# Kernel tuning notes

Measured on AMD Instinct MI355X. Metric: run time of the kernel, lower is better.

The kernel has to match this reference:

```python
import jax, jax.numpy as jnp
import numpy as np

VOCAB = 1024
HIDDEN = 64
BETA = 0.25


def setup_inputs() -> dict:
    key = jax.random.key(0)
    k1, k2 = jax.random.split(key)
    inputs = jax.random.normal(k1, (32, HIDDEN, 64, 64), dtype=jnp.float32)
    # nn.Embedding weight init: uniform(-1/vocab_size, 1/vocab_size)
    codebook = jax.random.uniform(k2, (VOCAB, HIDDEN), dtype=jnp.float32,
                                  minval=-1.0 / VOCAB, maxval=1.0 / VOCAB)
    return {"inputs": inputs, "codebook": codebook}


def reference(inputs, codebook):
    # NCHW -> NHWC
    x = jnp.transpose(inputs, (0, 2, 3, 1))  # [B,H,W,C]
    flat = x.reshape(-1, HIDDEN)             # [N,C]
    # squared L2 distances via the matmul expansion (as in the original)
    distances = (jnp.sum(flat ** 2, axis=1, keepdims=True)
                 + jnp.sum(codebook ** 2, axis=1)
                 - 2.0 * flat @ codebook.T)  # [N,V]
    idx = jnp.argmin(distances, axis=1)      # [N]
    one_hot = jax.nn.one_hot(idx, VOCAB, dtype=flat.dtype)  # [N,V]
    # one-hot @ codebook == gather; same math, efficient form
    quantized = codebook[idx].reshape(x.shape)  # [B,H,W,C]
    e_latent_loss = jnp.mean((jax.lax.stop_gradient(quantized) - x) ** 2)
    q_latent_loss = jnp.mean((quantized - jax.lax.stop_gradient(x)) ** 2)
    loss = q_latent_loss + BETA * e_latent_loss
    # straight-through estimator
    quantized_st = x + jax.lax.stop_gradient(quantized - x)
    avg_probs = jnp.mean(one_hot, axis=0)    # [V]
    perplexity = jnp.exp(-jnp.sum(avg_probs * jnp.log(avg_probs + 1e-10)))
    return (loss, jnp.transpose(quantized_st, (0, 3, 1, 2)), perplexity, one_hot)
```

## Files before the change

### kernel.cpp

```cpp
#include <hip/hip_runtime.h>

#define VOCAB 1024
#define HIDDEN 64
#define N_POS 131072
#define Q_ELEMS 8388608
#define BPOS 256
#define NBLK 512

#define OUT_Q_OFF 1
#define OUT_PPL_OFF 8388609
#define OUT_OH_OFF 8388610ULL

typedef __attribute__((ext_vector_type(8))) short short8v;
typedef __attribute__((ext_vector_type(4))) float f32x4;

__device__ __forceinline__ unsigned short bf16r(float f) {
    union { float f; unsigned u; } v; v.f = f;
    unsigned r = v.u + 0x7FFFu + ((v.u >> 16) & 1u);
    return (unsigned short)(r >> 16);
}
__device__ __forceinline__ float bf16tf(unsigned short h) {
    union { unsigned u; float f; } v; v.u = (unsigned)h << 16; return v.f;
}
__device__ __forceinline__ unsigned pk2(float a, float b) {
    return (unsigned)bf16r(a) | ((unsigned)bf16r(b) << 16);
}

__global__ __launch_bounds__(256) void vq_prep(
    const float* __restrict__ cb, unsigned* __restrict__ wsu,
    unsigned char* __restrict__ cbb, float* __restrict__ bsq)
{
    if (blockIdx.x == 4) {
        for (int i = threadIdx.x; i < 1089; i += 256) wsu[i] = 0u;
        return;
    }
    const int j = blockIdx.x * 256 + threadIdx.x;
    const float4* r = (const float4*)(cb + (size_t)j * HIDDEN);
    char* crow = (char*)cbb + (size_t)j * 128;
    const int swj = (j & 7) << 4;
    float ss = 0.f;
#pragma unroll
    for (int c4 = 0; c4 < 16; ++c4) {
        float4 v = r[c4];
        ss += v.x * v.x + v.y * v.y + v.z * v.z + v.w * v.w;
        *(uint2*)(crow + ((c4 * 8) ^ swj)) = make_uint2(pk2(v.x, v.y), pk2(v.z, v.w));
    }
    bsq[j] = -0.5f * ss;
}

__global__ __launch_bounds__(256, 3) void vq_main(
    const float* __restrict__ in, const unsigned char* __restrict__ cbb,
    const float* __restrict__ bsq, float* __restrict__ out,
    float* __restrict__ ws_loss, unsigned* __restrict__ counts,
    unsigned* __restrict__ ticket)
{
    __shared__ __align__(16) char smem[49216];
    unsigned*       xls32 = (unsigned*)smem;
    char*           cbs   = smem;
    unsigned short* qbuf  = (unsigned short*)smem;
    float*    bsqs  = (float*)(smem + 36864);
    float*    xsqp  = (float*)(smem + 40960);
    unsigned* hist  = (unsigned*)(smem + 45056);
    unsigned* lastf = (unsigned*)(smem + 49152);

    const int tid  = threadIdx.x;
    const int wid  = tid >> 6;
    const int lane = tid & 63;
    const int l15  = lane & 15;
    const int kg   = lane >> 4;
    const int kg4  = kg << 2, kgb = kg << 4;

    const int base = blockIdx.x * BPOS;
    const int b    = base >> 12;
    const int hw0  = base & 4095;
    const size_t B = (size_t)b * 262144;

    float* ohflat = out + OUT_OH_OFF + (size_t)base * VOCAB;

    for (int k = tid; k < VOCAB; k += 256) { hist[k] = 0u; bsqs[k] = bsq[k]; }

    {
        float4 sq = make_float4(0.f, 0.f, 0.f, 0.f);
        const float* bp = in + B + hw0 + 4 * lane;
#pragma unroll
        for (int c16 = 0; c16 < 16; c16 += 2) {
            const int c0 = wid * 16 + c16;
            float4 v0 = *(const float4*)(bp + (size_t)c0 * 4096);
            float4 v1 = *(const float4*)(bp + (size_t)(c0 + 1) * 4096);
            sq.x = fmaf(v0.x, v0.x, fmaf(v1.x, v1.x, sq.x));
            sq.y = fmaf(v0.y, v0.y, fmaf(v1.y, v1.y, sq.y));
            sq.z = fmaf(v0.z, v0.z, fmaf(v1.z, v1.z, sq.z));
            sq.w = fmaf(v0.w, v0.w, fmaf(v1.w, v1.w, sq.w));
            const int cc = c0 >> 1;
            xls32[(4 * lane + 0) * 36 + cc] = pk2(v0.x, v1.x);
            xls32[(4 * lane + 1) * 36 + cc] = pk2(v0.y, v1.y);
            xls32[(4 * lane + 2) * 36 + cc] = pk2(v0.z, v1.z);
            xls32[(4 * lane + 3) * 36 + cc] = pk2(v0.w, v1.w);
        }
        xsqp[wid * 256 + 4 * lane + 0] = sq.x;
        xsqp[wid * 256 + 4 * lane + 1] = sq.y;
        xsqp[wid * 256 + 4 * lane + 2] = sq.z;
        xsqp[wid * 256 + 4 * lane + 3] = sq.w;
    }
    __syncthreads();

    short8v xf[4][2];
#pragma unroll
    for (int bt = 0; bt < 4; ++bt)
#pragma unroll
    for (int kh = 0; kh < 2; ++kh)
        xf[bt][kh] = *(const short8v*)&xls32[(wid * 64 + bt * 16 + l15) * 36
                                            + kh * 16 + kg * 4];

    float rm[4];
#pragma unroll
    for (int bt = 0; bt < 4; ++bt) rm[bt] = -3.4e38f;

    for (int ch = 0; ch < 4; ++ch) {
        __syncthreads();
        {
            const uint4* src = (const uint4*)cbb + ch * 2048;
            uint4* dst = (uint4*)cbs;
#pragma unroll
            for (int k = 0; k < 8; ++k)
                dst[tid + k * 256] = src[tid + k * 256];
        }
        __syncthreads();

        for (int ct = 0; ct < 16; ++ct) {
            const int rbase = ct * 16 + l15;
            const char* arow = cbs + rbase * 128;
            const int sw = (rbase & 7) << 4;
            short8v a0 = *(const short8v*)(arow + (kgb ^ sw));
            short8v a1 = *(const short8v*)(arow + ((64 + kgb) ^ sw));
            f32x4 bsq4 = *(const f32x4*)&bsqs[ch * 256 + ct * 16 + kg4];
            const unsigned jb = (unsigned)(ch * 256 + ct * 16 + kg4);
#pragma unroll
            for (int bt = 0; bt < 4; ++bt) {
                f32x4 acc = bsq4;
                acc = __builtin_amdgcn_mfma_f32_16x16x32_bf16(a0, xf[bt][0], acc, 0, 0, 0);
                acc = __builtin_amdgcn_mfma_f32_16x16x32_bf16(a1, xf[bt][1], acc, 0, 0, 0);
#pragma unroll
                for (int r = 0; r < 4; ++r) {
                    unsigned pj = (__float_as_uint(acc[r]) & 0xFFFFFC00u) | (jb + r);
                    rm[bt] = fmaxf(rm[bt], __uint_as_float(pj));
                }
            }
        }
    }
    __syncthreads();

    float mred[4];
#pragma unroll
    for (int bt = 0; bt < 4; ++bt) {
        float m = rm[bt];
        m = fmaxf(m, __shfl_xor(m, 16));
        m = fmaxf(m, __shfl_xor(m, 32));
        mred[bt] = m;
    }
    const float m = kg == 0 ? mred[0] : kg == 1 ? mred[1]
                  : kg == 2 ? mred[2] : mred[3];
    const unsigned mu = __float_as_uint(m);
    const int   jf   = (int)(mu & 1023u);
    const float mval = __uint_as_float(mu & 0xFFFFFC00u);
    const float xs = xsqp[0 * 256 + tid] + xsqp[1 * 256 + tid]
                   + xsqp[2 * 256 + tid] + xsqp[3 * 256 + tid];
    float lsum = xs - 2.f * mval;

    ohflat[(size_t)tid * VOCAB + jf] = 1.0f;
    atomicAdd(&hist[jf], 1u);

    {
        const char* crow = (const char*)cbb + (size_t)jf * 128;
        const int swj = (jf & 7) << 4;
#pragma unroll
        for (int k = 0; k < 8; ++k) {
            uint4 u = *(const uint4*)(crow + ((k * 16) ^ swj));
            qbuf[(8 * k + 0) * 288 + tid] = (unsigned short)(u.x);
            qbuf[(8 * k + 1) * 288 + tid] = (unsigned short)(u.x >> 16);
            qbuf[(8 * k + 2) * 288 + tid] = (unsigned short)(u.y);
            qbuf[(8 * k + 3) * 288 + tid] = (unsigned short)(u.y >> 16);
            qbuf[(8 * k + 4) * 288 + tid] = (unsigned short)(u.z);
            qbuf[(8 * k + 5) * 288 + tid] = (unsigned short)(u.z >> 16);
            qbuf[(8 * k + 6) * 288 + tid] = (unsigned short)(u.w);
            qbuf[(8 * k + 7) * 288 + tid] = (unsigned short)(u.w >> 16);
        }
    }
    __syncthreads();

    for (int k = tid; k < VOCAB; k += 256) {
        unsigned h = hist[k];
        if (h) atomicAdd(&counts[k], h);
    }
#pragma unroll
    for (int off = 32; off; off >>= 1) lsum += __shfl_down(lsum, off);
    if (lane == 0) atomicAdd(&ws_loss[blockIdx.x & 63], lsum);

#pragma unroll 2
    for (int c16 = 0; c16 < 16; ++c16) {
        const int chn = wid * 16 + c16;
        const unsigned short* qr = qbuf + chn * 288;
        if (lane < 63) {
            const int mw = lane + 1;
            f32x4 v;
            v[0] = bf16tf(qr[4 * mw - 1]);
            v[1] = bf16tf(qr[4 * mw + 0]);
            v[2] = bf16tf(qr[4 * mw + 1]);
            v[3] = bf16tf(qr[4 * mw + 2]);
            __builtin_nontemporal_store(
                v, (f32x4*)(out + B + (size_t)chn * 4096 + hw0 + 4 * mw));
        } else {
            float* qp = out + OUT_Q_OFF + B + (size_t)chn * 4096 + hw0;
            __builtin_nontemporal_store(bf16tf(qr[0]),   &qp[0]);
            __builtin_nontemporal_store(bf16tf(qr[1]),   &qp[1]);
            __builtin_nontemporal_store(bf16tf(qr[2]),   &qp[2]);
            __builtin_nontemporal_store(bf16tf(qr[255]), &qp[255]);
        }
    }

    __syncthreads();
    if (tid == 0) *lastf = (atomicAdd(ticket, 1u) == NBLK - 1) ? 1u : 0u;
    __syncthreads();
    if (*lastf) {
        __threadfence();
        double s = 0.0;
        for (int k = tid; k < VOCAB; k += 256) {
            unsigned c = atomicAdd(&counts[k], 0u);
            double p = (double)c / (double)N_POS;
            s += -p * log(p + 1e-10);
        }
#pragma unroll
        for (int off = 32; off; off >>= 1) s += __shfl_down(s, off);
        double* red = (double*)hist;
        if ((tid & 63) == 0) red[tid >> 6] = s;
        __syncthreads();
        if (tid == 0)
            out[OUT_PPL_OFF] = (float)exp(red[0] + red[1] + red[2] + red[3]);
        if (tid < 64) {
            float l = atomicAdd(&ws_loss[tid], 0.0f);
#pragma unroll
            for (int off = 32; off; off >>= 1) l += __shfl_down(l, off);
            if (tid == 0) out[0] = l * 1.25f / (float)Q_ELEMS;
        }
    }
}

extern "C" void kernel_launch(void* const* d_in, const int* in_sizes, int n_in,
                              void* d_out, int out_size, void* d_ws, size_t ws_size,
                              hipStream_t stream) {
    const float* in = (const float*)d_in[0];
    const float* cb = (const float*)d_in[1];
    float* out = (float*)d_out;

    unsigned*      wsu     = (unsigned*)d_ws;
    float*         ws_loss = (float*)d_ws;
    unsigned*      counts  = (unsigned*)d_ws + 64;
    unsigned*      ticket  = (unsigned*)d_ws + 1088;
    unsigned char* cbb     = (unsigned char*)d_ws + 8192;
    float*         bsq     = (float*)((char*)d_ws + 139264);

    vq_prep<<<5, 256, 0, stream>>>(cb, wsu, cbb, bsq);
    vq_main<<<NBLK, 256, 0, stream>>>(in, cbb, bsq, out, ws_loss, counts, ticket);
}
```

Before: 61.33 us.

## Process two 256-position tiles per block to reuse each staged codebook chunk

Result: faster. 58.37 us (-4.8%).

```diff
diff --git a/kernel.cpp b/kernel.cpp
--- a/kernel.cpp
+++ b/kernel.cpp
@@ -4,8 +4,8 @@
 #define HIDDEN 64
 #define N_POS 131072
 #define Q_ELEMS 8388608
-#define BPOS 256
-#define NBLK 512
+#define BPOS 512
+#define NBLK 256
 
 #define OUT_Q_OFF 1
 #define OUT_PPL_OFF 8388609
@@ -79,42 +79,50 @@
 
     for (int k = tid; k < VOCAB; k += 256) { hist[k] = 0u; bsqs[k] = bsq[k]; }
 
-    {
-        float4 sq = make_float4(0.f, 0.f, 0.f, 0.f);
-        const float* bp = in + B + hw0 + 4 * lane;
-#pragma unroll
-        for (int c16 = 0; c16 < 16; c16 += 2) {
-            const int c0 = wid * 16 + c16;
-            float4 v0 = *(const float4*)(bp + (size_t)c0 * 4096);
-            float4 v1 = *(const float4*)(bp + (size_t)(c0 + 1) * 4096);
-            sq.x = fmaf(v0.x, v0.x, fmaf(v1.x, v1.x, sq.x));
-            sq.y = fmaf(v0.y, v0.y, fmaf(v1.y, v1.y, sq.y));
-            sq.z = fmaf(v0.z, v0.z, fmaf(v1.z, v1.z, sq.z));
-            sq.w = fmaf(v0.w, v0.w, fmaf(v1.w, v1.w, sq.w));
-            const int cc = c0 >> 1;
-            xls32[(4 * lane + 0) * 36 + cc] = pk2(v0.x, v1.x);
-            xls32[(4 * lane + 1) * 36 + cc] = pk2(v0.y, v1.y);
-            xls32[(4 * lane + 2) * 36 + cc] = pk2(v0.z, v1.z);
-            xls32[(4 * lane + 3) * 36 + cc] = pk2(v0.w, v1.w);
-        }
-        xsqp[wid * 256 + 4 * lane + 0] = sq.x;
-        xsqp[wid * 256 + 4 * lane + 1] = sq.y;
-        xsqp[wid * 256 + 4 * lane + 2] = sq.z;
-        xsqp[wid * 256 + 4 * lane + 3] = sq.w;
-    }
-    __syncthreads();
-
-    short8v xf[4][2];
-#pragma unroll
-    for (int bt = 0; bt < 4; ++bt)
-#pragma unroll
-    for (int kh = 0; kh < 2; ++kh)
-        xf[bt][kh] = *(const short8v*)&xls32[(wid * 64 + bt * 16 + l15) * 36
-                                            + kh * 16 + kg * 4];
-
-    float rm[4];
-#pragma unroll
-    for (int bt = 0; bt < 4; ++bt) rm[bt] = -3.4e38f;
+    short8v xf[2][4][2];
+    float xs[2];
+#pragma unroll
+    for (int t = 0; t < 2; ++t) {
+        __syncthreads();
+        {
+            float4 sq = make_float4(0.f, 0.f, 0.f, 0.f);
+            const float* bp = in + B + hw0 + t * 256 + 4 * lane;
+#pragma unroll
+            for (int c16 = 0; c16 < 16; c16 += 2) {
+                const int c0 = wid * 16 + c16;
+                float4 v0 = *(const float4*)(bp + (size_t)c0 * 4096);
+                float4 v1 = *(const float4*)(bp + (size_t)(c0 + 1) * 4096);
+                sq.x = fmaf(v0.x, v0.x, fmaf(v1.x, v1.x, sq.x));
+                sq.y = fmaf(v0.y, v0.y, fmaf(v1.y, v1.y, sq.y));
+                sq.z = fmaf(v0.z, v0.z, fmaf(v1.z, v1.z, sq.z));
+                sq.w = fmaf(v0.w, v0.w, fmaf(v1.w, v1.w, sq.w));
+                const int cc = c0 >> 1;
+                xls32[(4 * lane + 0) * 36 + cc] = pk2(v0.x, v1.x);
+                xls32[(4 * lane + 1) * 36 + cc] = pk2(v0.y, v1.y);
+                xls32[(4 * lane + 2) * 36 + cc] = pk2(v0.z, v1.z);
+                xls32[(4 * lane + 3) * 36 + cc] = pk2(v0.w, v1.w);
+            }
+            xsqp[wid * 256 + 4 * lane + 0] = sq.x;
+            xsqp[wid * 256 + 4 * lane + 1] = sq.y;
+            xsqp[wid * 256 + 4 * lane + 2] = sq.z;
+            xsqp[wid * 256 + 4 * lane + 3] = sq.w;
+        }
+        __syncthreads();
+#pragma unroll
+        for (int bt = 0; bt < 4; ++bt)
+#pragma unroll
+        for (int kh = 0; kh < 2; ++kh)
+            xf[t][bt][kh] = *(const short8v*)&xls32[(wid * 64 + bt * 16 + l15) * 36
+                                                    + kh * 16 + kg * 4];
+        xs[t] = xsqp[0 * 256 + tid] + xsqp[1 * 256 + tid]
+              + xsqp[2 * 256 + tid] + xsqp[3 * 256 + tid];
+    }
+
+    float rm[2][4];
+#pragma unroll
+    for (int t = 0; t < 2; ++t)
+#pragma unroll
+    for (int bt = 0; bt < 4; ++bt) rm[t][bt] = -3.4e38f;
 
     for (int ch = 0; ch < 4; ++ch) {
         __syncthreads();
@@ -136,85 +144,93 @@
             f32x4 bsq4 = *(const f32x4*)&bsqs[ch * 256 + ct * 16 + kg4];
             const unsigned jb = (unsigned)(ch * 256 + ct * 16 + kg4);
 #pragma unroll
+            for (int t = 0; t < 2; ++t)
+#pragma unroll
             for (int bt = 0; bt < 4; ++bt) {
                 f32x4 acc = bsq4;
-                acc = __builtin_amdgcn_mfma_f32_16x16x32_bf16(a0, xf[bt][0], acc, 0, 0, 0);
-                acc = __builtin_amdgcn_mfma_f32_16x16x32_bf16(a1, xf[bt][1], acc, 0, 0, 0);
+                acc = __builtin_amdgcn_mfma_f32_16x16x32_bf16(a0, xf[t][bt][0], acc, 0, 0, 0);
+                acc = __builtin_amdgcn_mfma_f32_16x16x32_bf16(a1, xf[t][bt][1], acc, 0, 0, 0);
 #pragma unroll
                 for (int r = 0; r < 4; ++r) {
                     unsigned pj = (__float_as_uint(acc[r]) & 0xFFFFFC00u) | (jb + r);
-                    rm[bt] = fmaxf(rm[bt], __uint_as_float(pj));
+                    rm[t][bt] = fmaxf(rm[t][bt], __uint_as_float(pj));
                 }
             }
         }
     }
     __syncthreads();
 
-    float mred[4];
-#pragma unroll
-    for (int bt = 0; bt < 4; ++bt) {
-        float m = rm[bt];
-        m = fmaxf(m, __shfl_xor(m, 16));
-        m = fmaxf(m, __shfl_xor(m, 32));
-        mred[bt] = m;
-    }
-    const float m = kg == 0 ? mred[0] : kg == 1 ? mred[1]
-                  : kg == 2 ? mred[2] : mred[3];
-    const unsigned mu = __float_as_uint(m);
-    const int   jf   = (int)(mu & 1023u);
-    const float mval = __uint_as_float(mu & 0xFFFFFC00u);
-    const float xs = xsqp[0 * 256 + tid] + xsqp[1 * 256 + tid]
-                   + xsqp[2 * 256 + tid] + xsqp[3 * 256 + tid];
-    float lsum = xs - 2.f * mval;
-
-    ohflat[(size_t)tid * VOCAB + jf] = 1.0f;
-    atomicAdd(&hist[jf], 1u);
-
-    {
-        const char* crow = (const char*)cbb + (size_t)jf * 128;
-        const int swj = (jf & 7) << 4;
-#pragma unroll
-        for (int k = 0; k < 8; ++k) {
-            uint4 u = *(const uint4*)(crow + ((k * 16) ^ swj));
-            qbuf[(8 * k + 0) * 288 + tid] = (unsigned short)(u.x);
-            qbuf[(8 * k + 1) * 288 + tid] = (unsigned short)(u.x >> 16);
-            qbuf[(8 * k + 2) * 288 + tid] = (unsigned short)(u.y);
-            qbuf[(8 * k + 3) * 288 + tid] = (unsigned short)(u.y >> 16);
-            qbuf[(8 * k + 4) * 288 + tid] = (unsigned short)(u.z);
-            qbuf[(8 * k + 5) * 288 + tid] = (unsigned short)(u.z >> 16);
-            qbuf[(8 * k + 6) * 288 + tid] = (unsigned short)(u.w);
-            qbuf[(8 * k + 7) * 288 + tid] = (unsigned short)(u.w >> 16);
-        }
-    }
-    __syncthreads();
-
-    for (int k = tid; k < VOCAB; k += 256) {
-        unsigned h = hist[k];
-        if (h) atomicAdd(&counts[k], h);
+    int jf[2];
+    float lsum = 0.f;
+#pragma unroll
+    for (int t = 0; t < 2; ++t) {
+        float mred[4];
+#pragma unroll
+        for (int bt = 0; bt < 4; ++bt) {
+            float m = rm[t][bt];
+            m = fmaxf(m, __shfl_xor(m, 16));
+            m = fmaxf(m, __shfl_xor(m, 32));
+            mred[bt] = m;
+        }
+        const float m = kg == 0 ? mred[0] : kg == 1 ? mred[1]
+                      : kg == 2 ? mred[2] : mred[3];
+        const unsigned mu = __float_as_uint(m);
+        jf[t] = (int)(mu & 1023u);
+        const float mval = __uint_as_float(mu & 0xFFFFFC00u);
+        lsum += xs[t] - 2.f * mval;
+        ohflat[(size_t)(t * 256 + tid) * VOCAB + jf[t]] = 1.0f;
+        atomicAdd(&hist[jf[t]], 1u);
     }
 #pragma unroll
     for (int off = 32; off; off >>= 1) lsum += __shfl_down(lsum, off);
     if (lane == 0) atomicAdd(&ws_loss[blockIdx.x & 63], lsum);
 
+#pragma unroll
+    for (int t = 0; t < 2; ++t) {
+        __syncthreads();
+        {
+            const char* crow = (const char*)cbb + (size_t)jf[t] * 128;
+            const int swj = (jf[t] & 7) << 4;
+#pragma unroll
+            for (int k = 0; k < 8; ++k) {
+                uint4 u = *(const uint4*)(crow + ((k * 16) ^ swj));
+                qbuf[(8 * k + 0) * 288 + tid] = (unsigned short)(u.x);
+                qbuf[(8 * k + 1) * 288 + tid] = (unsigned short)(u.x >> 16);
+                qbuf[(8 * k + 2) * 288 + tid] = (unsigned short)(u.y);
+                qbuf[(8 * k + 3) * 288 + tid] = (unsigned short)(u.y >> 16);
+                qbuf[(8 * k + 4) * 288 + tid] = (unsigned short)(u.z);
+                qbuf[(8 * k + 5) * 288 + tid] = (unsigned short)(u.z >> 16);
+                qbuf[(8 * k + 6) * 288 + tid] = (unsigned short)(u.w);
+                qbuf[(8 * k + 7) * 288 + tid] = (unsigned short)(u.w >> 16);
+            }
+        }
+        if (t == 0) {
+            for (int k = tid; k < VOCAB; k += 256) {
+                unsigned h = hist[k];
+                if (h) atomicAdd(&counts[k], h);
+            }
+        }
+        __syncthreads();
+
 #pragma unroll 2
-    for (int c16 = 0; c16 < 16; ++c16) {
-        const int chn = wid * 16 + c16;
-        const unsigned short* qr = qbuf + chn * 288;
-        if (lane < 63) {
-            const int mw = lane + 1;
-            f32x4 v;
-            v[0] = bf16tf(qr[4 * mw - 1]);
-            v[1] = bf16tf(qr[4 * mw + 0]);
-            v[2] = bf16tf(qr[4 * mw + 1]);
-            v[3] = bf16tf(qr[4 * mw + 2]);
-            __builtin_nontemporal_store(
-                v, (f32x4*)(out + B + (size_t)chn * 4096 + hw0 + 4 * mw));
-        } else {
-            float* qp = out + OUT_Q_OFF + B + (size_t)chn * 4096 + hw0;
-            __builtin_nontemporal_store(bf16tf(qr[0]),   &qp[0]);
-            __builtin_nontemporal_store(bf16tf(qr[1]),   &qp[1]);
-            __builtin_nontemporal_store(bf16tf(qr[2]),   &qp[2]);
-            __builtin_nontemporal_store(bf16tf(qr[255]), &qp[255]);
+        for (int c16 = 0; c16 < 16; ++c16) {
+            const int chn = wid * 16 + c16;
+            const unsigned short* qr = qbuf + chn * 288;
+            float* cbase = out + B + (size_t)chn * 4096 + hw0 + t * 256;
+            if (lane < 63) {
+                const int mw = lane + 1;
+                f32x4 v;
+                v[0] = bf16tf(qr[4 * mw - 1]);
+                v[1] = bf16tf(qr[4 * mw + 0]);
+                v[2] = bf16tf(qr[4 * mw + 1]);
+                v[3] = bf16tf(qr[4 * mw + 2]);
+                __builtin_nontemporal_store(v, (f32x4*)(cbase + 4 * mw));
+            } else {
+                __builtin_nontemporal_store(bf16tf(qr[0]),   cbase + 1);
+                __builtin_nontemporal_store(bf16tf(qr[1]),   cbase + 2);
+                __builtin_nontemporal_store(bf16tf(qr[2]),   cbase + 3);
+                __builtin_nontemporal_store(bf16tf(qr[255]), cbase + 256);
+            }
         }
     }
 
```
